# Optimization experiments

Measured on AMD Instinct MI355X. Metric: run time of the kernel, lower is better.

The kernel has to match this reference:

```python
import jax, jax.numpy as jnp
import numpy as np

B, N, F, E = 256, 784, 1, 6272   # batch, nodes, in-features, edges
C = 32                            # GraphConv channels
H = 512                           # fc1 hidden units
N_OUT = 10


def setup_inputs() -> dict:
    key = jax.random.key(0)
    ks = jax.random.split(key, 12)
    x = jax.random.normal(ks[0], (B, N, F), dtype=jnp.float32)
    edge_row = jax.random.randint(ks[1], (E,), 0, N, dtype=jnp.int32)
    edge_col = jax.random.randint(ks[2], (E,), 0, N, dtype=jnp.int32)
    edge_val = jax.random.uniform(ks[3], (E,), dtype=jnp.float32)
    # GraphConv weights (Glorot-ish scale)
    W1 = jax.random.normal(ks[4], (F, C), dtype=jnp.float32) * 0.5
    b1 = jnp.zeros((C,), dtype=jnp.float32)
    W2 = jax.random.normal(ks[5], (C, C), dtype=jnp.float32) * 0.18
    b2 = jnp.zeros((C,), dtype=jnp.float32)
    # MLP head
    Wf1 = jax.random.normal(ks[6], (N * C, H), dtype=jnp.float32) * 0.01
    bf1 = jnp.zeros((H,), dtype=jnp.float32)
    Wf2 = jax.random.normal(ks[7], (H, N_OUT), dtype=jnp.float32) * 0.04
    bf2 = jnp.zeros((N_OUT,), dtype=jnp.float32)
    return {"x": x, "edge_row": edge_row, "edge_col": edge_col, "edge_val": edge_val,
            "W1": W1, "b1": b1, "W2": W2, "b2": b2,
            "Wf1": Wf1, "bf1": bf1, "Wf2": Wf2, "bf2": bf2}


def _spmm(h, row, col, val):
    # h: [B, N, C]; sparse fltr (COO) @ h per batch element
    msg = jnp.swapaxes(h[:, col, :], 0, 1) * val[:, None, None]      # [E, B, C]
    agg = jax.ops.segment_sum(msg, row, num_segments=N)              # [N, B, C]
    return jnp.swapaxes(agg, 0, 1)                                   # [B, N, C]


def reference(x, edge_row, edge_col, edge_val, W1, b1, W2, b2, Wf1, bf1, Wf2, bf2):
    # GraphConv 1: elu(fltr @ x @ W1 + b1)
    h = jax.nn.elu(_spmm(x, edge_row, edge_col, edge_val) @ W1 + b1)
    # GraphConv 2
    h = jax.nn.elu(_spmm(h, edge_row, edge_col, edge_val) @ W2 + b2)
    # Flatten -> Dense(512, relu) -> Dense(10, softmax)
    flat = h.reshape(B, N * C)
    z = jax.nn.relu(flat @ Wf1 + bf1)
    return jax.nn.softmax(z @ Wf2 + bf2, axis=-1)
```

## Files before the change

kernel.cpp:

```cpp
#include <hip/hip_runtime.h>
#include <hip/hip_bf16.h>

#define B_ 256
#define N_ 784
#define E_ 6272
#define C_ 32
#define H_ 512
#define NK 25088
#define BC 8192
#define S_SPLIT 28

typedef __attribute__((ext_vector_type(8))) short short8;
typedef __attribute__((ext_vector_type(4))) float f32x4;

__device__ __forceinline__ float elu1(float v) {
  return v > 0.f ? v : (__expf(v) - 1.f);
}

__device__ __forceinline__ unsigned short bf16b(float v) {
  __hip_bfloat16 h = __float2bfloat16(v);
  return *reinterpret_cast<unsigned short*>(&h);
}

__device__ __forceinline__ unsigned int pk2(float lo, float hi) {
  return (unsigned int)bf16b(lo) | ((unsigned int)bf16b(hi) << 16);
}

__device__ __forceinline__ void acc2(unsigned u, float val, float& a0, float& a1) {
  float lo = __uint_as_float(u << 16);
  float hi = __uint_as_float(u & 0xffff0000u);
  a0 = fmaf(val, lo, a0);
  a1 = fmaf(val, hi, a1);
}

__global__ __launch_bounds__(1024) void k_prep(
    const int* __restrict__ erow, const int* __restrict__ ecol,
    const float* __restrict__ eval, const float* __restrict__ x,
    const float* __restrict__ Wf1,
    int* __restrict__ row_ptr, int* __restrict__ col_s, float* __restrict__ val_s,
    float* __restrict__ xT, __hip_bfloat16* __restrict__ wf1t) {
  const int t = threadIdx.x;
  if (blockIdx.x == 0) {
    __shared__ int cnt[N_];
    __shared__ int off[N_];
    __shared__ int bufA[1024];
    __shared__ int bufB[1024];
    if (t < N_) cnt[t] = 0;
    __syncthreads();
    for (int e = t; e < E_; e += 1024) atomicAdd(&cnt[erow[e]], 1);
    __syncthreads();
    bufA[t] = (t < N_) ? cnt[t] : 0;
    __syncthreads();
    int* src = bufA; int* dst = bufB;
    for (int d = 1; d < 1024; d <<= 1) {
      int v = src[t];
      if (t >= d) v += src[t - d];
      dst[t] = v;
      __syncthreads();
      int* tmp = src; src = dst; dst = tmp;
    }
    if (t < N_) {
      int ex = src[t] - cnt[t];
      off[t] = ex;
      row_ptr[t] = ex;
    }
    if (t == 0) row_ptr[N_] = E_;
    __syncthreads();
    for (int e = t; e < E_; e += 1024) {
      int r = erow[e];
      int p = atomicAdd(&off[r], 1);
      col_s[p] = ecol[e];
      val_s[p] = eval[e];
    }
  } else if (blockIdx.x <= 200) {
    __shared__ float tile[32][33];
    int bid = blockIdx.x - 1;
    int n0 = (bid % 25) * 32, b0 = (bid / 25) * 32;
    int ni = t & 31, bi = t >> 5;
    int n = n0 + ni;
    if (n < N_) tile[ni][bi] = x[(b0 + bi) * N_ + n];
    __syncthreads();
    int nj = t >> 5, bj = t & 31;
    int nw = n0 + nj;
    if (nw < N_) xT[nw * B_ + b0 + bj] = tile[nj][bj];
  } else {
    __shared__ float tile[64][65];
    int bid = blockIdx.x - 201;
    int k0 = (bid % 392) * 64, n0 = (bid / 392) * 64;
#pragma unroll
    for (int it = 0; it < 4; ++it) {
      int idx = it * 1024 + t;
      int k = idx >> 6, n = idx & 63;
      tile[k][n] = Wf1[(size_t)(k0 + k) * H_ + n0 + n];
    }
    __syncthreads();
#pragma unroll
    for (int it = 0; it < 2; ++it) {
      int idx = it * 1024 + t;
      int n = idx >> 5, kp = idx & 31;
      unsigned int v = pk2(tile[2 * kp][n], tile[2 * kp + 1][n]);
      *reinterpret_cast<unsigned int*>(
          wf1t + (size_t)(n0 + n) * NK + k0 + 2 * kp) = v;
    }
  }
}

__global__ __launch_bounds__(256) void k_gc1(
    const float* __restrict__ xT, const int* __restrict__ row_ptr,
    const int* __restrict__ col_s, const float* __restrict__ val_s,
    const float* __restrict__ W1, const float* __restrict__ b1,
    __hip_bfloat16* __restrict__ h1) {
  __shared__ int lc[64];
  __shared__ float lv[64];
  int n = blockIdx.x, t = threadIdx.x;
  int e0 = row_ptr[n], deg = row_ptr[n + 1] - e0;
  float agg = 0.f;
  for (int base = 0; base < deg; base += 64) {
    int m = min(64, deg - base);
    __syncthreads();
    if (t < m) { lc[t] = col_s[e0 + base + t]; lv[t] = val_s[e0 + base + t]; }
    __syncthreads();
    int e = 0;
    for (; e + 4 <= m; e += 4) {
      float x0 = xT[lc[e + 0] * B_ + t];
      float x1 = xT[lc[e + 1] * B_ + t];
      float x2 = xT[lc[e + 2] * B_ + t];
      float x3 = xT[lc[e + 3] * B_ + t];
      agg = fmaf(lv[e + 0], x0, agg);
      agg = fmaf(lv[e + 1], x1, agg);
      agg = fmaf(lv[e + 2], x2, agg);
      agg = fmaf(lv[e + 3], x3, agg);
    }
    for (; e < m; ++e)
      agg = fmaf(lv[e], xT[lc[e] * B_ + t], agg);
  }
  union { unsigned int u[16]; uint4 v[4]; } ob;
#pragma unroll
  for (int c = 0; c < C_; c += 2) {
    float o0 = elu1(fmaf(agg, W1[c], b1[c]));
    float o1 = elu1(fmaf(agg, W1[c + 1], b1[c + 1]));
    ob.u[c >> 1] = pk2(o0, o1);
  }
  uint4* dst = reinterpret_cast<uint4*>(h1 + (size_t)n * BC + t * C_);
#pragma unroll
  for (int j = 0; j < 4; ++j) dst[j] = ob.v[j];
}

__global__ __launch_bounds__(128) void k_gc2(
    const __hip_bfloat16* __restrict__ h1, const int* __restrict__ row_ptr,
    const int* __restrict__ col_s, const float* __restrict__ val_s,
    const float* __restrict__ W2, const float* __restrict__ b2,
    __hip_bfloat16* __restrict__ flat) {
  __shared__ int lc[64];
  __shared__ float lv[64];
  int n = blockIdx.x, t = threadIdx.x;
  int tb = blockIdx.y * 128 + t;
  int e0 = row_ptr[n], deg = row_ptr[n + 1] - e0;
  float acc[C_];
#pragma unroll
  for (int c = 0; c < C_; ++c) acc[c] = 0.f;

#define ACC16(v0, v1, v2, v3, val) do {                                       \
    acc2(v0.x, val, acc[0], acc[1]);  acc2(v0.y, val, acc[2], acc[3]);        \
    acc2(v0.z, val, acc[4], acc[5]);  acc2(v0.w, val, acc[6], acc[7]);        \
    acc2(v1.x, val, acc[8], acc[9]);  acc2(v1.y, val, acc[10], acc[11]);      \
    acc2(v1.z, val, acc[12], acc[13]); acc2(v1.w, val, acc[14], acc[15]);     \
    acc2(v2.x, val, acc[16], acc[17]); acc2(v2.y, val, acc[18], acc[19]);     \
    acc2(v2.z, val, acc[20], acc[21]); acc2(v2.w, val, acc[22], acc[23]);     \
    acc2(v3.x, val, acc[24], acc[25]); acc2(v3.y, val, acc[26], acc[27]);     \
    acc2(v3.z, val, acc[28], acc[29]); acc2(v3.w, val, acc[30], acc[31]);     \
  } while (0)

  for (int base = 0; base < deg; base += 64) {
    int m = min(64, deg - base);
    __syncthreads();
    if (t < m && t < 64) { lc[t] = col_s[e0 + base + t]; lv[t] = val_s[e0 + base + t]; }
    __syncthreads();
    int e = 0;
    for (; e + 4 <= m; e += 4) {
      const uint4* p0 = reinterpret_cast<const uint4*>(h1 + (size_t)lc[e + 0] * BC + tb * C_);
      const uint4* p1 = reinterpret_cast<const uint4*>(h1 + (size_t)lc[e + 1] * BC + tb * C_);
      const uint4* p2 = reinterpret_cast<const uint4*>(h1 + (size_t)lc[e + 2] * BC + tb * C_);
      const uint4* p3 = reinterpret_cast<const uint4*>(h1 + (size_t)lc[e + 3] * BC + tb * C_);
      uint4 a0 = p0[0], a1 = p0[1], a2 = p0[2], a3 = p0[3];
      uint4 b0 = p1[0], b1 = p1[1], b2v = p1[2], b3 = p1[3];
      uint4 c0 = p2[0], c1 = p2[1], c2 = p2[2], c3 = p2[3];
      uint4 d0 = p3[0], d1 = p3[1], d2 = p3[2], d3 = p3[3];
      float va = lv[e], vb = lv[e + 1], vc = lv[e + 2], vd = lv[e + 3];
      ACC16(a0, a1, a2, a3, va);
      ACC16(b0, b1, b2v, b3, vb);
      ACC16(c0, c1, c2, c3, vc);
      ACC16(d0, d1, d2, d3, vd);
    }
    for (; e < m; ++e) {
      const uint4* p0 = reinterpret_cast<const uint4*>(h1 + (size_t)lc[e] * BC + tb * C_);
      uint4 a0 = p0[0], a1 = p0[1], a2 = p0[2], a3 = p0[3];
      ACC16(a0, a1, a2, a3, lv[e]);
    }
  }
#undef ACC16

  union { unsigned int u[16]; uint4 v[4]; } ob;
#pragma unroll
  for (int c2 = 0; c2 < C_; c2 += 2) {
    float o0 = b2[c2], o1 = b2[c2 + 1];
#pragma unroll
    for (int c = 0; c < C_; ++c) {
      o0 = fmaf(acc[c], W2[c * C_ + c2], o0);
      o1 = fmaf(acc[c], W2[c * C_ + c2 + 1], o1);
    }
    ob.u[c2 >> 1] = pk2(elu1(o0), elu1(o1));
  }
  uint4* dst = reinterpret_cast<uint4*>(flat + (size_t)tb * NK + n * C_);
#pragma unroll
  for (int j = 0; j < 4; ++j) dst[j] = ob.v[j];
}

__global__ __launch_bounds__(256, 2) void k_fc1(
    const __hip_bfloat16* __restrict__ flat, const __hip_bfloat16* __restrict__ wf1t,
    float* __restrict__ partial) {
  __shared__ unsigned char lds[3 * 24576];
  int raw = blockIdx.x;
  int bid = (raw & 7) * 56 + (raw >> 3);
  int s = bid >> 4, r16 = bid & 15;
  int m0 = (r16 & 1) * 128;
  int n0 = (r16 >> 1) * 64;
  int k0 = s * 896;
  int tid = threadIdx.x;
  int w = tid >> 6, l = tid & 63;
  int r = l & 15, g = l >> 4;

  const __hip_bfloat16* src[6];
  int ldsoff[6];
#pragma unroll
  for (int j = 0; j < 6; ++j) {
    int reg = w * 6 + j;
    ldsoff[j] = reg * 1024 + l * 16;
    if (reg < 16) {
      int fmg = reg >> 1, ks = reg & 1;
      src[j] = flat + (size_t)(m0 + fmg * 16 + r) * NK + (k0 + ks * 32 + g * 8);
    } else {
      int fng = (reg - 16) >> 1, ks = reg & 1;
      src[j] = wf1t + (size_t)(n0 + fng * 16 + r) * NK + (k0 + ks * 32 + g * 8);
    }
  }

  f32x4 acc[4][2];
#pragma unroll
  for (int i = 0; i < 4; ++i)
#pragma unroll
    for (int j = 0; j < 2; ++j) acc[i][j] = (f32x4){0.f, 0.f, 0.f, 0.f};

#define GLOAD_LDS(gp, lp)                                                     \
  __builtin_amdgcn_global_load_lds(                                           \
      (const __attribute__((address_space(1))) unsigned int*)(gp),            \
      (__attribute__((address_space(3))) unsigned int*)(lp), 16, 0, 0)
#define STAGE(t, buf) do {                                                    \
    _Pragma("unroll")                                                         \
    for (int j = 0; j < 6; ++j)                                               \
      GLOAD_LDS(src[j] + (t) * 64, &lds[(buf) * 24576 + ldsoff[j]]);          \
  } while (0)
#define VWAIT(n) do {                                                         \
    asm volatile("s_waitcnt vmcnt(%0)" :: "n"(n) : "memory");                 \
    __builtin_amdgcn_sched_barrier(0);                                        \
  } while (0)
#define BAR() do {                                                            \
    __builtin_amdgcn_s_barrier();                                             \
    __builtin_amdgcn_sched_barrier(0);                                        \
  } while (0)
#define COMPUTE(buf) do {                                                     \
    const unsigned char* bb = &lds[(buf) * 24576];                            \
    short8 af[4][2], bf[2][2];                                                \
    _Pragma("unroll")                                                         \
    for (int fm = 0; fm < 4; ++fm)                                            \
      _Pragma("unroll")                                                       \
      for (int ks = 0; ks < 2; ++ks)                                          \
        af[fm][ks] = *reinterpret_cast<const short8*>(                        \
            bb + (((4 * (w & 1) + fm) * 2 + ks) << 10) + l * 16);             \
    _Pragma("unroll")                                                         \
    for (int fn = 0; fn < 2; ++fn)                                            \
      _Pragma("unroll")                                                       \
      for (int ks = 0; ks < 2; ++ks)                                          \
        bf[fn][ks] = *reinterpret_cast<const short8*>(                        \
            bb + ((16 + (2 * (w >> 1) + fn) * 2 + ks) << 10) + l * 16);       \
    _Pragma("unroll")                                                         \
    for (int ks = 0; ks < 2; ++ks)                                            \
      _Pragma("unroll")                                                       \
      for (int fn = 0; fn < 2; ++fn)                                          \
        _Pragma("unroll")                                                     \
        for (int fm = 0; fm < 4; ++fm)                                        \
          acc[fm][fn] = __builtin_amdgcn_mfma_f32_16x16x32_bf16(              \
              af[fm][ks], bf[fn][ks], acc[fm][fn], 0, 0, 0);                  \
  } while (0)
#define STEP(t) do {                                                          \
    VWAIT((t) < 13 ? 6 : 0);                                                  \
    BAR();                                                                    \
    if ((t) + 2 <= 13) STAGE((t) + 2, ((t) + 2) % 3);                         \
    COMPUTE((t) % 3);                                                         \
  } while (0)

  STAGE(0, 0);
  STAGE(1, 1);
  STEP(0);  STEP(1);  STEP(2);  STEP(3);  STEP(4);  STEP(5);  STEP(6);
  STEP(7);  STEP(8);  STEP(9);  STEP(10); STEP(11); STEP(12); STEP(13);

#undef GLOAD_LDS
#undef STAGE
#undef VWAIT
#undef BAR
#undef COMPUTE
#undef STEP

  int wm = (w & 1) * 64, wn = (w >> 1) * 32;
  float* p = partial + (size_t)s * (256 * 512);
#pragma unroll
  for (int fm = 0; fm < 4; ++fm)
#pragma unroll
    for (int fn = 0; fn < 2; ++fn)
#pragma unroll
      for (int q = 0; q < 4; ++q) {
        int m = m0 + wm + fm * 16 + g * 4 + q;
        int n = n0 + wn + fn * 16 + r;
        p[m * 512 + n] = acc[fm][fn][q];
      }
}

__global__ __launch_bounds__(512) void k_head(
    const float* __restrict__ partial, const float* __restrict__ bf1,
    const float* __restrict__ Wf2, const float* __restrict__ bf2,
    float* __restrict__ out) {
  __shared__ float red[8][12];
  int b = blockIdx.x;
  int t = threadIdx.x;
  float v = bf1[t];
#pragma unroll
  for (int s = 0; s < S_SPLIT; ++s)
    v += partial[(size_t)s * (256 * 512) + b * 512 + t];
  v = fmaxf(v, 0.f);
  float pacc[10];
#pragma unroll
  for (int j = 0; j < 10; ++j) pacc[j] = v * Wf2[t * 10 + j];
#pragma unroll
  for (int j = 0; j < 10; ++j)
#pragma unroll
    for (int d = 32; d > 0; d >>= 1)
      pacc[j] += __shfl_down(pacc[j], d);
  int wv = t >> 6, ln = t & 63;
  if (ln == 0) {
#pragma unroll
    for (int j = 0; j < 10; ++j) red[wv][j] = pacc[j];
  }
  __syncthreads();
  if (t == 0) {
    float lg[10];
    float m = -1e30f;
#pragma unroll
    for (int j = 0; j < 10; ++j) {
      float z = bf2[j];
#pragma unroll
      for (int wq = 0; wq < 8; ++wq) z += red[wq][j];
      lg[j] = z;
      m = fmaxf(m, z);
    }
    float sum = 0.f;
#pragma unroll
    for (int j = 0; j < 10; ++j) { lg[j] = __expf(lg[j] - m); sum += lg[j]; }
    float inv = 1.f / sum;
#pragma unroll
    for (int j = 0; j < 10; ++j) out[b * 10 + j] = lg[j] * inv;
  }
}

extern "C" void kernel_launch(void* const* d_in, const int* in_sizes, int n_in,
                              void* d_out, int out_size, void* d_ws, size_t ws_size,
                              hipStream_t stream) {
  const float* x    = (const float*)d_in[0];
  const int*   erow = (const int*)d_in[1];
  const int*   ecol = (const int*)d_in[2];
  const float* ev   = (const float*)d_in[3];
  const float* W1   = (const float*)d_in[4];
  const float* b1   = (const float*)d_in[5];
  const float* W2   = (const float*)d_in[6];
  const float* b2   = (const float*)d_in[7];
  const float* Wf1  = (const float*)d_in[8];
  const float* bf1  = (const float*)d_in[9];
  const float* Wf2  = (const float*)d_in[10];
  const float* bf2  = (const float*)d_in[11];
  float* out = (float*)d_out;

  const size_t partial_bytes = (size_t)S_SPLIT * 256 * 512 * 4;
  const size_t flat_bytes    = (size_t)B_ * NK * 2;
  const size_t wf1t_bytes    = (size_t)H_ * NK * 2;

  char* ws = (char*)d_ws;
  float* partial = (float*)ws;
  float* xT = (float*)ws;
  __hip_bfloat16* h1 = (__hip_bfloat16*)(ws + 802816);
  __hip_bfloat16* flat = (__hip_bfloat16*)(ws + partial_bytes);
  __hip_bfloat16* wf1t = (__hip_bfloat16*)(ws + partial_bytes + flat_bytes);
  char* tail = ws + partial_bytes + flat_bytes + wf1t_bytes;
  int*   row_ptr = (int*)tail;
  int*   col_s   = (int*)(tail + 3152);
  float* val_s   = (float*)(tail + 3152 + E_ * 4);

  hipLaunchKernelGGL(k_prep, dim3(1 + 200 + 392 * 8), dim3(1024), 0, stream,
                     erow, ecol, ev, x, Wf1, row_ptr, col_s, val_s, xT, wf1t);
  hipLaunchKernelGGL(k_gc1, dim3(N_), dim3(256), 0, stream,
                     xT, row_ptr, col_s, val_s, W1, b1, h1);
  hipLaunchKernelGGL(k_gc2, dim3(N_, 2), dim3(128), 0, stream,
                     h1, row_ptr, col_s, val_s, W2, b2, flat);
  hipLaunchKernelGGL(k_fc1, dim3(S_SPLIT * 16), dim3(256), 0, stream,
                     flat, wf1t, partial);
  hipLaunchKernelGGL(k_head, dim3(B_), dim3(512), 0, stream,
                     partial, bf1, Wf2, bf2, out);
}
```

Measured before the change: 92.04 us.

## Replace sparse GraphConv2 gather with dense bf16 adjacency MFMA GEMM per batch

The second graph convolution no longer gathers sparse neighbours per node. It builds a dense 784x800 bf16 adjacency matrix and runs a per-batch MFMA GEMM against a transposed h1 layout, with the W2 projection and ELU fused into the epilogue. The first layer is now computed per batch in LDS, and the Wf1 transpose is split between the prep and h1T kernels so it overlaps other work. The adjacency is about 99% zeros, so this spends much more arithmetic to gain regular matrix-core throughput. Duplicate edges are accumulated in bf16, which adds some rounding error.

```diff
diff --git a/kernel.cpp b/kernel.cpp
--- a/kernel.cpp
+++ b/kernel.cpp
@@ -7,7 +7,7 @@
 #define C_ 32
 #define H_ 512
 #define NK 25088
-#define BC 8192
+#define KP 800
 #define S_SPLIT 28
 
 typedef __attribute__((ext_vector_type(8))) short short8;
@@ -26,19 +26,11 @@
   return (unsigned int)bf16b(lo) | ((unsigned int)bf16b(hi) << 16);
 }
 
-__device__ __forceinline__ void acc2(unsigned u, float val, float& a0, float& a1) {
-  float lo = __uint_as_float(u << 16);
-  float hi = __uint_as_float(u & 0xffff0000u);
-  a0 = fmaf(val, lo, a0);
-  a1 = fmaf(val, hi, a1);
-}
-
 __global__ __launch_bounds__(1024) void k_prep(
     const int* __restrict__ erow, const int* __restrict__ ecol,
-    const float* __restrict__ eval, const float* __restrict__ x,
-    const float* __restrict__ Wf1,
+    const float* __restrict__ eval, const float* __restrict__ Wf1,
     int* __restrict__ row_ptr, int* __restrict__ col_s, float* __restrict__ val_s,
-    float* __restrict__ xT, __hip_bfloat16* __restrict__ wf1t) {
+    __hip_bfloat16* __restrict__ adj, __hip_bfloat16* __restrict__ wf1t) {
   const int t = threadIdx.x;
   if (blockIdx.x == 0) {
     __shared__ int cnt[N_];
@@ -72,21 +64,16 @@
       col_s[p] = ecol[e];
       val_s[p] = eval[e];
     }
-  } else if (blockIdx.x <= 200) {
-    __shared__ float tile[32][33];
-    int bid = blockIdx.x - 1;
-    int n0 = (bid % 25) * 32, b0 = (bid / 25) * 32;
-    int ni = t & 31, bi = t >> 5;
-    int n = n0 + ni;
-    if (n < N_) tile[ni][bi] = x[(b0 + bi) * N_ + n];
-    __syncthreads();
-    int nj = t >> 5, bj = t & 31;
-    int nw = n0 + nj;
-    if (nw < N_) xT[nw * B_ + b0 + bj] = tile[nj][bj];
+  } else if (blockIdx.x <= 77) {
+    size_t off16 = ((size_t)(blockIdx.x - 1) * 1024 + t) * 16;
+    if (off16 < (size_t)N_ * KP * 2) {
+      int4 z = {0, 0, 0, 0};
+      *reinterpret_cast<int4*>(reinterpret_cast<char*>(adj) + off16) = z;
+    }
   } else {
     __shared__ float tile[64][65];
-    int bid = blockIdx.x - 201;
-    int k0 = (bid % 392) * 64, n0 = (bid / 392) * 64;
+    int bid = blockIdx.x - 78;
+    int k0 = (bid % 196) * 64, n0 = (bid / 196) * 64;
 #pragma unroll
     for (int it = 0; it < 4; ++it) {
       int idx = it * 1024 + t;
@@ -105,115 +92,205 @@
   }
 }
 
-__global__ __launch_bounds__(256) void k_gc1(
-    const float* __restrict__ xT, const int* __restrict__ row_ptr,
+__global__ __launch_bounds__(256) void k_h1T(
+    const float* __restrict__ x, const int* __restrict__ row_ptr,
     const int* __restrict__ col_s, const float* __restrict__ val_s,
     const float* __restrict__ W1, const float* __restrict__ b1,
-    __hip_bfloat16* __restrict__ h1) {
-  __shared__ int lc[64];
-  __shared__ float lv[64];
-  int n = blockIdx.x, t = threadIdx.x;
-  int e0 = row_ptr[n], deg = row_ptr[n + 1] - e0;
-  float agg = 0.f;
-  for (int base = 0; base < deg; base += 64) {
-    int m = min(64, deg - base);
-    __syncthreads();
-    if (t < m) { lc[t] = col_s[e0 + base + t]; lv[t] = val_s[e0 + base + t]; }
-    __syncthreads();
-    int e = 0;
-    for (; e + 4 <= m; e += 4) {
-      float x0 = xT[lc[e + 0] * B_ + t];
-      float x1 = xT[lc[e + 1] * B_ + t];
-      float x2 = xT[lc[e + 2] * B_ + t];
-      float x3 = xT[lc[e + 3] * B_ + t];
-      agg = fmaf(lv[e + 0], x0, agg);
-      agg = fmaf(lv[e + 1], x1, agg);
-      agg = fmaf(lv[e + 2], x2, agg);
-      agg = fmaf(lv[e + 3], x3, agg);
-    }
-    for (; e < m; ++e)
-      agg = fmaf(lv[e], xT[lc[e] * B_ + t], agg);
-  }
-  union { unsigned int u[16]; uint4 v[4]; } ob;
-#pragma unroll
-  for (int c = 0; c < C_; c += 2) {
-    float o0 = elu1(fmaf(agg, W1[c], b1[c]));
-    float o1 = elu1(fmaf(agg, W1[c + 1], b1[c + 1]));
-    ob.u[c >> 1] = pk2(o0, o1);
-  }
-  uint4* dst = reinterpret_cast<uint4*>(h1 + (size_t)n * BC + t * C_);
-#pragma unroll
-  for (int j = 0; j < 4; ++j) dst[j] = ob.v[j];
-}
-
-__global__ __launch_bounds__(128) void k_gc2(
-    const __hip_bfloat16* __restrict__ h1, const int* __restrict__ row_ptr,
-    const int* __restrict__ col_s, const float* __restrict__ val_s,
+    const float* __restrict__ Wf1, __hip_bfloat16* __restrict__ adj,
+    __hip_bfloat16* __restrict__ wf1t, __hip_bfloat16* __restrict__ h1T) {
+  __shared__ float sm[64 * 65];
+  int bid = blockIdx.x, t = threadIdx.x;
+  if (bid < B_) {
+    int b = bid;
+    float* xls = sm;
+    float* aggls = sm + N_;
+    for (int i = t; i < N_; i += 256) xls[i] = x[(size_t)b * N_ + i];
+    __syncthreads();
+    for (int i = t; i < N_; i += 256) {
+      int e0 = row_ptr[i], e1 = row_ptr[i + 1];
+      float a = 0.f;
+      for (int e = e0; e < e1; ++e) a = fmaf(val_s[e], xls[col_s[e]], a);
+      aggls[i] = a;
+    }
+    __syncthreads();
+#pragma unroll
+    for (int c = 0; c < C_; ++c) {
+      __hip_bfloat16* rowp = h1T + (size_t)(b * C_ + c) * KP;
+      float wc = W1[c], bc = b1[c];
+      for (int i = t; i < KP / 2; i += 256) {
+        int n = 2 * i;
+        float v0 = (n < N_) ? elu1(fmaf(aggls[n], wc, bc)) : 0.f;
+        float v1 = (n + 1 < N_) ? elu1(fmaf(aggls[n + 1], wc, bc)) : 0.f;
+        *reinterpret_cast<unsigned int*>(rowp + n) = pk2(v0, v1);
+      }
+    }
+  } else if (bid < B_ + 4) {
+    int n = (bid - B_) * 256 + t;
+    if (n < N_) {
+      int e0 = row_ptr[n], e1 = row_ptr[n + 1];
+      for (int e = e0; e < e1; ++e) {
+        __hip_bfloat16* p = adj + (size_t)n * KP + col_s[e];
+        float cur = __bfloat162float(*p);
+        *p = __float2bfloat16(cur + val_s[e]);
+      }
+    }
+  } else {
+    int bid2 = bid - (B_ + 4);
+    int k0 = 12544 + (bid2 % 196) * 64, n0 = (bid2 / 196) * 64;
+    float (*tile)[65] = reinterpret_cast<float(*)[65]>(sm);
+#pragma unroll
+    for (int it = 0; it < 16; ++it) {
+      int idx = it * 256 + t;
+      int kk = idx >> 6, nn = idx & 63;
+      tile[kk][nn] = Wf1[(size_t)(k0 + kk) * H_ + n0 + nn];
+    }
+    __syncthreads();
+#pragma unroll
+    for (int it = 0; it < 8; ++it) {
+      int idx = it * 256 + t;
+      int nn = idx >> 5, kp = idx & 31;
+      unsigned int v = pk2(tile[2 * kp][nn], tile[2 * kp + 1][nn]);
+      *reinterpret_cast<unsigned int*>(
+          wf1t + (size_t)(n0 + nn) * NK + k0 + 2 * kp) = v;
+    }
+  }
+}
+
+__global__ __launch_bounds__(448, 1) void k_gemm2(
+    const __hip_bfloat16* __restrict__ adj, const __hip_bfloat16* __restrict__ h1T,
     const float* __restrict__ W2, const float* __restrict__ b2,
     __hip_bfloat16* __restrict__ flat) {
-  __shared__ int lc[64];
-  __shared__ float lv[64];
-  int n = blockIdx.x, t = threadIdx.x;
-  int tb = blockIdx.y * 128 + t;
-  int e0 = row_ptr[n], deg = row_ptr[n + 1] - e0;
-  float acc[C_];
-#pragma unroll
-  for (int c = 0; c < C_; ++c) acc[c] = 0.f;
-
-#define ACC16(v0, v1, v2, v3, val) do {                                       \
-    acc2(v0.x, val, acc[0], acc[1]);  acc2(v0.y, val, acc[2], acc[3]);        \
-    acc2(v0.z, val, acc[4], acc[5]);  acc2(v0.w, val, acc[6], acc[7]);        \
-    acc2(v1.x, val, acc[8], acc[9]);  acc2(v1.y, val, acc[10], acc[11]);      \
-    acc2(v1.z, val, acc[12], acc[13]); acc2(v1.w, val, acc[14], acc[15]);     \
-    acc2(v2.x, val, acc[16], acc[17]); acc2(v2.y, val, acc[18], acc[19]);     \
-    acc2(v2.z, val, acc[20], acc[21]); acc2(v2.w, val, acc[22], acc[23]);     \
-    acc2(v3.x, val, acc[24], acc[25]); acc2(v3.y, val, acc[26], acc[27]);     \
-    acc2(v3.z, val, acc[28], acc[29]); acc2(v3.w, val, acc[30], acc[31]);     \
-  } while (0)
-
-  for (int base = 0; base < deg; base += 64) {
-    int m = min(64, deg - base);
-    __syncthreads();
-    if (t < m && t < 64) { lc[t] = col_s[e0 + base + t]; lv[t] = val_s[e0 + base + t]; }
-    __syncthreads();
-    int e = 0;
-    for (; e + 4 <= m; e += 4) {
-      const uint4* p0 = reinterpret_cast<const uint4*>(h1 + (size_t)lc[e + 0] * BC + tb * C_);
-      const uint4* p1 = reinterpret_cast<const uint4*>(h1 + (size_t)lc[e + 1] * BC + tb * C_);
-      const uint4* p2 = reinterpret_cast<const uint4*>(h1 + (size_t)lc[e + 2] * BC + tb * C_);
-      const uint4* p3 = reinterpret_cast<const uint4*>(h1 + (size_t)lc[e + 3] * BC + tb * C_);
-      uint4 a0 = p0[0], a1 = p0[1], a2 = p0[2], a3 = p0[3];
-      uint4 b0 = p1[0], b1 = p1[1], b2v = p1[2], b3 = p1[3];
-      uint4 c0 = p2[0], c1 = p2[1], c2 = p2[2], c3 = p2[3];
-      uint4 d0 = p3[0], d1 = p3[1], d2 = p3[2], d3 = p3[3];
-      float va = lv[e], vb = lv[e + 1], vc = lv[e + 2], vd = lv[e + 3];
-      ACC16(a0, a1, a2, a3, va);
-      ACC16(b0, b1, b2v, b3, vb);
-      ACC16(c0, c1, c2, c3, vc);
-      ACC16(d0, d1, d2, d3, vd);
-    }
-    for (; e < m; ++e) {
-      const uint4* p0 = reinterpret_cast<const uint4*>(h1 + (size_t)lc[e] * BC + tb * C_);
-      uint4 a0 = p0[0], a1 = p0[1], a2 = p0[2], a3 = p0[3];
-      ACC16(a0, a1, a2, a3, lv[e]);
-    }
-  }
-#undef ACC16
-
-  union { unsigned int u[16]; uint4 v[4]; } ob;
-#pragma unroll
-  for (int c2 = 0; c2 < C_; c2 += 2) {
-    float o0 = b2[c2], o1 = b2[c2 + 1];
-#pragma unroll
-    for (int c = 0; c < C_; ++c) {
-      o0 = fmaf(acc[c], W2[c * C_ + c2], o0);
-      o1 = fmaf(acc[c], W2[c * C_ + c2 + 1], o1);
-    }
-    ob.u[c2 >> 1] = pk2(elu1(o0), elu1(o1));
-  }
-  uint4* dst = reinterpret_cast<uint4*>(flat + (size_t)tb * NK + n * C_);
-#pragma unroll
-  for (int j = 0; j < 4; ++j) dst[j] = ob.v[j];
+  __shared__ alignas(16) unsigned char lds[117248];
+  int b = blockIdx.x;
+  int tid = threadIdx.x;
+  int w = tid >> 6, l = tid & 63;
+  int r = l & 15, g = l >> 4;
+  int wbase = w * 112;
+
+  float* w2ls = reinterpret_cast<float*>(lds + 112896);
+  float* b2ls = reinterpret_cast<float*>(lds + 117120);
+  for (int i = tid; i < 1024; i += 448)
+    w2ls[(i >> 5) * 33 + (i & 31)] = W2[i];
+  if (tid < 32) b2ls[tid] = b2[tid];
+
+#define GLOAD_LDS(gp, lp)                                                     \
+  __builtin_amdgcn_global_load_lds(                                           \
+      (const __attribute__((address_space(1))) unsigned int*)(gp),            \
+      (__attribute__((address_space(3))) unsigned int*)(lp), 16, 0, 0)
+
+#pragma unroll
+  for (int i = 0; i < 8; ++i) {
+    int f = w + 7 * i;
+    if (f < 50) {
+      int fn = f / 25, ks = f - fn * 25;
+      GLOAD_LDS(h1T + (size_t)(b * C_ + fn * 16 + r) * KP + ks * 32 + g * 8,
+                lds + f * 1024 + l * 16);
+    }
+  }
+  __syncthreads();
+
+  const __hip_bfloat16* pa[7];
+#pragma unroll
+  for (int fm = 0; fm < 7; ++fm)
+    pa[fm] = adj + (size_t)(wbase + fm * 16 + r) * KP + g * 8;
+
+  f32x4 acc[7][2];
+#pragma unroll
+  for (int i = 0; i < 7; ++i)
+#pragma unroll
+    for (int j = 0; j < 2; ++j) acc[i][j] = (f32x4){0.f, 0.f, 0.f, 0.f};
+
+  int4 va[3][7];
+
+#define ALOAD(dst, ptr, imm)                                                  \
+  asm volatile("global_load_dwordx4 %0, %1, off offset:%2"                    \
+               : "=v"(dst) : "v"(ptr), "n"(imm))
+#define AISSUE(s) do {                                                        \
+    _Pragma("unroll")                                                         \
+    for (int fm = 0; fm < 7; ++fm)                                            \
+      ALOAD(va[(s) % 3][fm], pa[fm], (s) * 64);                               \
+  } while (0)
+#define AWAIT(n) do {                                                         \
+    asm volatile("s_waitcnt vmcnt(%0)" :: "n"(n) : "memory");                 \
+    __builtin_amdgcn_sched_barrier(0);                                        \
+  } while (0)
+#define ASTEP(t) do {                                                         \
+    if ((t) + 2 < 25) AISSUE((t) + 2);                                        \
+    AWAIT((t) <= 22 ? 14 : ((t) == 23 ? 7 : 0));                              \
+    short8 _b0 = *reinterpret_cast<const short8*>(lds + (t) * 1024 + l * 16); \
+    short8 _b1 = *reinterpret_cast<const short8*>(lds + (25 + (t)) * 1024 + l * 16); \
+    _Pragma("unroll")                                                         \
+    for (int fm = 0; fm < 7; ++fm) {                                          \
+      short8 _a = *reinterpret_cast<short8*>(&va[(t) % 3][fm]);               \
+      acc[fm][0] = __builtin_amdgcn_mfma_f32_16x16x32_bf16(_a, _b0, acc[fm][0], 0, 0, 0); \
+      acc[fm][1] = __builtin_amdgcn_mfma_f32_16x16x32_bf16(_a, _b1, acc[fm][1], 0, 0, 0); \
+    }                                                                         \
+  } while (0)
+
+  AISSUE(0); AISSUE(1);
+  ASTEP(0);  ASTEP(1);  ASTEP(2);  ASTEP(3);  ASTEP(4);
+  ASTEP(5);  ASTEP(6);  ASTEP(7);  ASTEP(8);  ASTEP(9);
+  ASTEP(10); ASTEP(11); ASTEP(12); ASTEP(13); ASTEP(14);
+  ASTEP(15); ASTEP(16); ASTEP(17); ASTEP(18); ASTEP(19);
+  ASTEP(20); ASTEP(21); ASTEP(22); ASTEP(23); ASTEP(24);
+
+#undef ALOAD
+#undef AISSUE
+#undef AWAIT
+#undef ASTEP
+#undef GLOAD_LDS
+
+  __syncthreads();
+
+  float* epf = reinterpret_cast<float*>(lds + w * 16128);
+#pragma unroll
+  for (int fm = 0; fm < 7; ++fm)
+#pragma unroll
+    for (int fn = 0; fn < 2; ++fn)
+#pragma unroll
+      for (int q = 0; q < 4; ++q)
+        epf[fm * 576 + (g * 4 + q) * 36 + fn * 16 + r] = acc[fm][fn][q];
+
+  int row = l >> 2, cq = l & 3;
+  float o[7][8];
+#pragma unroll
+  for (int fm = 0; fm < 7; ++fm)
+#pragma unroll
+    for (int j = 0; j < 8; ++j) o[fm][j] = b2ls[cq * 8 + j];
+
+#pragma unroll
+  for (int cb = 0; cb < 4; ++cb) {
+    float w2r[8][8];
+#pragma unroll
+    for (int cc = 0; cc < 8; ++cc)
+#pragma unroll
+      for (int j = 0; j < 8; ++j)
+        w2r[cc][j] = w2ls[(cb * 8 + cc) * 33 + cq * 8 + j];
+#pragma unroll
+    for (int fm = 0; fm < 7; ++fm) {
+      f32x4 a0 = *reinterpret_cast<f32x4*>(&epf[fm * 576 + row * 36 + cb * 8]);
+      f32x4 a1 = *reinterpret_cast<f32x4*>(&epf[fm * 576 + row * 36 + cb * 8 + 4]);
+#pragma unroll
+      for (int cc = 0; cc < 4; ++cc)
+#pragma unroll
+        for (int j = 0; j < 8; ++j)
+          o[fm][j] = fmaf(a0[cc], w2r[cc][j], o[fm][j]);
+#pragma unroll
+      for (int cc = 0; cc < 4; ++cc)
+#pragma unroll
+        for (int j = 0; j < 8; ++j)
+          o[fm][j] = fmaf(a1[cc], w2r[4 + cc][j], o[fm][j]);
+    }
+  }
+
+#pragma unroll
+  for (int fm = 0; fm < 7; ++fm) {
+    int dest = wbase + fm * 16 + row;
+    union { unsigned short u[8]; int4 v; } ob;
+#pragma unroll
+    for (int j = 0; j < 8; ++j) ob.u[j] = bf16b(elu1(o[fm][j]));
+    *reinterpret_cast<int4*>(flat + (size_t)b * NK + dest * C_ + cq * 8) = ob.v;
+  }
 }
 
 __global__ __launch_bounds__(256, 2) void k_fc1(
@@ -391,24 +468,26 @@
   const size_t partial_bytes = (size_t)S_SPLIT * 256 * 512 * 4;
   const size_t flat_bytes    = (size_t)B_ * NK * 2;
   const size_t wf1t_bytes    = (size_t)H_ * NK * 2;
+  const size_t h1t_bytes     = (size_t)B_ * C_ * KP * 2;
+  const size_t adj_bytes     = (size_t)N_ * KP * 2;
 
   char* ws = (char*)d_ws;
-  float* partial = (float*)ws;
-  float* xT = (float*)ws;
-  __hip_bfloat16* h1 = (__hip_bfloat16*)(ws + 802816);
-  __hip_bfloat16* flat = (__hip_bfloat16*)(ws + partial_bytes);
-  __hip_bfloat16* wf1t = (__hip_bfloat16*)(ws + partial_bytes + flat_bytes);
-  char* tail = ws + partial_bytes + flat_bytes + wf1t_bytes;
+  float* partial          = (float*)ws;
+  __hip_bfloat16* flat    = (__hip_bfloat16*)(ws + partial_bytes);
+  __hip_bfloat16* wf1t    = (__hip_bfloat16*)(ws + partial_bytes + flat_bytes);
+  __hip_bfloat16* h1T     = (__hip_bfloat16*)(ws + partial_bytes + flat_bytes + wf1t_bytes);
+  __hip_bfloat16* adj     = (__hip_bfloat16*)(ws + partial_bytes + flat_bytes + wf1t_bytes + h1t_bytes);
+  char* tail = ws + partial_bytes + flat_bytes + wf1t_bytes + h1t_bytes + adj_bytes;
   int*   row_ptr = (int*)tail;
   int*   col_s   = (int*)(tail + 3152);
   float* val_s   = (float*)(tail + 3152 + E_ * 4);
 
-  hipLaunchKernelGGL(k_prep, dim3(1 + 200 + 392 * 8), dim3(1024), 0, stream,
-                     erow, ecol, ev, x, Wf1, row_ptr, col_s, val_s, xT, wf1t);
-  hipLaunchKernelGGL(k_gc1, dim3(N_), dim3(256), 0, stream,
-                     xT, row_ptr, col_s, val_s, W1, b1, h1);
-  hipLaunchKernelGGL(k_gc2, dim3(N_, 2), dim3(128), 0, stream,
-                     h1, row_ptr, col_s, val_s, W2, b2, flat);
+  hipLaunchKernelGGL(k_prep, dim3(1 + 77 + 1568), dim3(1024), 0, stream,
+                     erow, ecol, ev, Wf1, row_ptr, col_s, val_s, adj, wf1t);
+  hipLaunchKernelGGL(k_h1T, dim3(B_ + 4 + 1568), dim3(256), 0, stream,
+                     x, row_ptr, col_s, val_s, W1, b1, Wf1, adj, wf1t, h1T);
+  hipLaunchKernelGGL(k_gemm2, dim3(B_), dim3(448), 0, stream,
+                     adj, h1T, W2, b2, flat);
   hipLaunchKernelGGL(k_fc1, dim3(S_SPLIT * 16), dim3(256), 0, stream,
                      flat, wf1t, partial);
   hipLaunchKernelGGL(k_head, dim3(B_), dim3(512), 0, stream,
```

After: 152.1 us. 65.3% more time.
